# Kernel tuning notes

Measured on AMD Instinct MI355X. Metric: run time of the kernel, lower is better.

The kernel has to match this reference:

```python
import jax, jax.numpy as jnp
import numpy as np

STRIDE = 1
PAD = 1


def setup_inputs() -> dict:
    key = jax.random.key(0)
    k1, k2, k3 = jax.random.split(key, 3)
    # Single image (C_in, H, W) as in the original unbatched HETensor list layout
    x = jax.random.normal(k1, (256, 512, 512), dtype=jnp.float32)
    # Weights in HWIO layout (kh, kw, C_in, C_out) matching load_weights' expected shape
    W = jax.random.normal(k2, (3, 3, 256, 256), dtype=jnp.float32) * 0.02
    b = jax.random.normal(k3, (256,), dtype=jnp.float32)
    return {"x": x, "W": W, "b": b}


def reference(x, W, b):
    # Zero-pad then convolve; out_h = ceil((H + 2*PAD - kh + 1)/STRIDE) == lax conv output for stride 1
    out = jax.lax.conv_general_dilated(
        x[None],                      # [1, C_in, H, W]
        W,                            # [kh, kw, C_in, C_out]
        window_strides=(STRIDE, STRIDE),
        padding=[(PAD, PAD), (PAD, PAD)],
        dimension_numbers=("NCHW", "HWIO", "NCHW"),
    )
    return out[0] + b[:, None, None]  # [C_out, H, W]
```

## Files before the change

### kernel.cpp

```cpp
#include <hip/hip_runtime.h>
#include <hip/hip_bf16.h>


typedef __attribute__((ext_vector_type(8))) short bf16x8;
typedef __attribute__((ext_vector_type(4))) float floatx4;

#define HWSZ 262144
#define CIN  256
#define HH   512
#define WWD  512

__device__ __forceinline__ void async_copy16(const void* g, void* l) {
  __builtin_amdgcn_global_load_lds(
      (const __attribute__((address_space(1))) void*)g,
      (__attribute__((address_space(3))) void*)l, 16, 0, 0);
}

__global__ __launch_bounds__(256) void convert_x(
    const float* __restrict__ x, __hip_bfloat16* __restrict__ xt)
{
  const int b = blockIdx.x;
  const int h = b >> 1;
  const int w = ((b & 1) << 8) + threadIdx.x;
  const float* xp = x + (size_t)h * WWD + w;
#pragma unroll 2
  for (int cg = 0; cg < 32; ++cg) {
    const float* s = xp + (size_t)(cg << 3) * HWSZ;
    unsigned int q[4];
#pragma unroll
    for (int k = 0; k < 4; ++k) {
      float f0 = s[(size_t)(2 * k) * HWSZ];
      float f1 = s[(size_t)(2 * k + 1) * HWSZ];
      __hip_bfloat16 b0 = __float2bfloat16(f0);
      __hip_bfloat16 b1 = __float2bfloat16(f1);
      q[k] = (unsigned int)*(const unsigned short*)&b0 |
             ((unsigned int)*(const unsigned short*)&b1 << 16);
    }
    uint4 v;
    v.x = q[0]; v.y = q[1]; v.z = q[2]; v.w = q[3];
    *(uint4*)&xt[(((size_t)h * 32 + cg) << 12) + ((size_t)w << 3)] = v;
  }
}

__global__ __launch_bounds__(256) void convert_w(
    const float* __restrict__ Wf, __hip_bfloat16* __restrict__ wt,
    __hip_bfloat16* __restrict__ zb)
{
  const int idx = blockIdx.x * 256 + threadIdx.x;
  const int ci = idx & 255;
  const int co = (idx >> 8) & 255;
  const int kk = idx >> 16;
  wt[(((size_t)(kk * 32 + (ci >> 3)) * 256 + co) << 3) + (ci & 7)] =
      __float2bfloat16(Wf[((size_t)(kk * 256 + ci) << 8) + co]);
  if (idx < 64) zb[idx] = __float2bfloat16(0.0f);
}

__global__ __launch_bounds__(256, 3) void conv_mfma(
    const __hip_bfloat16* __restrict__ xt,
    const __hip_bfloat16* __restrict__ wt,
    const float* __restrict__ bias,
    float* __restrict__ out,
    const __hip_bfloat16* __restrict__ zb)
{
  __shared__ __align__(16) __hip_bfloat16 As[3 * 128 * 32];
  __shared__ __align__(16) __hip_bfloat16 Bs[130 * 32];

  const int b     = blockIdx.x;
  const int xcd   = b & 7;
  const int local = b >> 3;
  const int h     = (xcd << 6) + (local >> 3);
  const int rem   = local & 7;
  const int cot   = rem >> 2;
  const int wti   = rem & 3;
  const int w0   = wti << 7;
  const int co0  = cot << 7;
  const int t    = threadIdx.x;
  const int lane = t & 63;
  const int wave = t >> 6;
  const int wm   = wave & 1;
  const int wn   = wave >> 1;
  const int mcol = lane & 15;
  const int krow = lane >> 4;


  floatx4 acc[4][4];
#pragma unroll
  for (int mi = 0; mi < 4; ++mi)
#pragma unroll
    for (int ni = 0; ni < 4; ++ni) {
      floatx4 z = {0.f, 0.f, 0.f, 0.f};
      acc[mi][ni] = z;
    }

  for (int kh = 0; kh < 3; ++kh) {
    const int hp = h + kh - 1;
    const bool hok = (unsigned)hp < (unsigned)HH;
    const __hip_bfloat16* xrow = xt + ((size_t)hp << 17);

    for (int ci0 = 0; ci0 < CIN; ci0 += 32) {
      const int cg0 = ci0 >> 3;
      __syncthreads();
#pragma unroll
      for (int rnd = 0; rnd < 6; ++rnd) {
        int c  = rnd * 256 + t;
        int kw = c >> 9;
        int m  = (c >> 2) & 127;
        int j  = c & 3;
        int js = j ^ ((m >> 1) & 3);
        const __hip_bfloat16* g =
            wt + (((size_t)((kh * 3 + kw) * 32 + cg0 + js)) << 11) + ((co0 + m) << 3);
        async_copy16(g, &As[c << 3]);
      }
#pragma unroll
      for (int rnd = 0; rnd < 2; ++rnd) {
        int c = rnd * 256 + t;
        int r = c >> 2;
        int j = c & 3;
        int js = j ^ ((r >> 1) & 3);
        int wp = w0 - 1 + r;
        const __hip_bfloat16* g = (hok && (unsigned)wp < (unsigned)WWD)
            ? xrow + ((size_t)(cg0 + js) << 12) + (wp << 3)
            : zb + (js << 3);
        async_copy16(g, &Bs[c << 3]);
      }
      if (t < 8) {
        int c = 512 + t;
        int r = c >> 2;
        int j = c & 3;
        int js = j ^ ((r >> 1) & 3);
        int wp = w0 - 1 + r;
        const __hip_bfloat16* g = (hok && (unsigned)wp < (unsigned)WWD)
            ? xrow + ((size_t)(cg0 + js) << 12) + (wp << 3)
            : zb + (js << 3);
        async_copy16(g, &Bs[c << 3]);
      }
      __syncthreads();

#pragma unroll
      for (int kw = 0; kw < 3; ++kw) {
        bf16x8 af[4], bfr[4];
#pragma unroll
        for (int mi = 0; mi < 4; ++mi) {
          int row = wm * 64 + mi * 16 + mcol;
          af[mi] = *(const bf16x8*)&As[(kw << 12) + (row << 5) +
                                       ((krow ^ ((row >> 1) & 3)) << 3)];
        }
#pragma unroll
        for (int ni = 0; ni < 4; ++ni) {
          int r = wn * 64 + ni * 16 + mcol + kw;
          bfr[ni] = *(const bf16x8*)&Bs[(r << 5) +
                                        ((krow ^ ((r >> 1) & 3)) << 3)];
        }
#pragma unroll
        for (int mi = 0; mi < 4; ++mi)
#pragma unroll
          for (int ni = 0; ni < 4; ++ni)
            acc[mi][ni] = __builtin_amdgcn_mfma_f32_16x16x32_bf16(
                af[mi], bfr[ni], acc[mi][ni], 0, 0, 0);
      }
    }
  }

  const size_t outrow = (size_t)h * WWD;
#pragma unroll
  for (int mi = 0; mi < 4; ++mi) {
#pragma unroll
    for (int r = 0; r < 4; ++r) {
      int co = co0 + wm * 64 + mi * 16 + krow * 4 + r;
      float bv = bias[co];
      float* op = out + (size_t)co * HWSZ + outrow + w0 + wn * 64 + mcol;
#pragma unroll
      for (int ni = 0; ni < 4; ++ni)
        op[ni * 16] = acc[mi][ni][r] + bv;
    }
  }
}

__global__ __launch_bounds__(256) void conv_naive(
    const float* __restrict__ x, const float* __restrict__ Wf,
    const float* __restrict__ bias, float* __restrict__ out)
{
  size_t idx = (size_t)blockIdx.x * 256 + threadIdx.x;
  int w  = (int)(idx & 511);
  int h  = (int)((idx >> 9) & 511);
  int co = (int)(idx >> 18);
  float acc = bias[co];
  for (int kh = 0; kh < 3; ++kh) {
    int hp = h + kh - 1;
    if ((unsigned)hp >= 512u) continue;
    for (int kw = 0; kw < 3; ++kw) {
      int wp = w + kw - 1;
      if ((unsigned)wp >= 512u) continue;
      const float* wcol = Wf + ((size_t)(kh * 3 + kw) << 16) + co;
      const float* xpix = x + (size_t)hp * 512 + wp;
      for (int ci = 0; ci < 256; ++ci)
        acc += xpix[(size_t)ci * HWSZ] * wcol[(size_t)ci << 8];
    }
  }
  out[idx] = acc;
}

extern "C" void kernel_launch(void* const* d_in, const int* in_sizes, int n_in,
                              void* d_out, int out_size, void* d_ws, size_t ws_size,
                              hipStream_t stream) {
  const float* x    = (const float*)d_in[0];
  const float* Wf   = (const float*)d_in[1];
  const float* bias = (const float*)d_in[2];
  float* out = (float*)d_out;

  const size_t xt_bytes = (size_t)HH * WWD * CIN * 2;
  const size_t wt_bytes = (size_t)9 * 256 * 256 * 2;
  const size_t need = xt_bytes + wt_bytes + 256;

  if (ws_size >= need) {
    __hip_bfloat16* xt = (__hip_bfloat16*)d_ws;
    __hip_bfloat16* wt = (__hip_bfloat16*)((char*)d_ws + xt_bytes);
    __hip_bfloat16* zb = (__hip_bfloat16*)((char*)d_ws + xt_bytes + wt_bytes);
    convert_x<<<1024, 256, 0, stream>>>(x, xt);
    convert_w<<<2304, 256, 0, stream>>>(Wf, wt, zb);
    conv_mfma<<<4096, 256, 0, stream>>>(xt, wt, bias, out, zb);
  } else {
    conv_naive<<<262144, 256, 0, stream>>>(x, Wf, bias, out);
  }
}
```

Before: 809.4 us.

## Double-buffer conv MFMA LDS tiles and regroup bf16 layout into 32-channel chunks

Reworks the implicit-GEMM convolution so global-to-LDS async copies for the next (kh, channel-chunk) stage are issued while the current stage's MFMAs run, using two LDS buffers and one barrier per stage. The x and weight bf16 intermediate layouts are regrouped so each pixel/output channel stores 32 contiguous channels, which makes global loads contiguous. The two halo columns are now loaded directly into registers and patched into the B fragments rather than staged in LDS. LDS use doubles and occupancy is lowered to 2 blocks per CU, trading latency hiding through occupancy for explicit prefetch.

```diff
diff --git a/kernel.cpp b/kernel.cpp
--- a/kernel.cpp
+++ b/kernel.cpp
@@ -19,26 +19,33 @@
 __global__ __launch_bounds__(256) void convert_x(
     const float* __restrict__ x, __hip_bfloat16* __restrict__ xt)
 {
-  const int b = blockIdx.x;
-  const int h = b >> 1;
-  const int w = ((b & 1) << 8) + threadIdx.x;
-  const float* xp = x + (size_t)h * WWD + w;
+  const int b  = blockIdx.x;
+  const int h  = b >> 1;
+  const int wh = (b & 1) << 8;
+  const int t  = threadIdx.x;
+  const int q  = t >> 2;
+  const int j  = t & 3;
+  const float* xbase = x + (size_t)h * WWD;
 #pragma unroll 2
-  for (int cg = 0; cg < 32; ++cg) {
-    const float* s = xp + (size_t)(cg << 3) * HWSZ;
-    unsigned int q[4];
-#pragma unroll
-    for (int k = 0; k < 4; ++k) {
-      float f0 = s[(size_t)(2 * k) * HWSZ];
-      float f1 = s[(size_t)(2 * k + 1) * HWSZ];
-      __hip_bfloat16 b0 = __float2bfloat16(f0);
-      __hip_bfloat16 b1 = __float2bfloat16(f1);
-      q[k] = (unsigned int)*(const unsigned short*)&b0 |
-             ((unsigned int)*(const unsigned short*)&b1 << 16);
-    }
-    uint4 v;
-    v.x = q[0]; v.y = q[1]; v.z = q[2]; v.w = q[3];
-    *(uint4*)&xt[(((size_t)h * 32 + cg) << 12) + ((size_t)w << 3)] = v;
+  for (int cg4 = 0; cg4 < 8; ++cg4) {
+#pragma unroll
+    for (int pass = 0; pass < 4; ++pass) {
+      int w = wh + pass * 64 + q;
+      const float* s = xbase + (size_t)(cg4 * 32 + j * 8) * HWSZ + w;
+      unsigned int qw[4];
+#pragma unroll
+      for (int k = 0; k < 4; ++k) {
+        float f0 = s[(size_t)(2 * k) * HWSZ];
+        float f1 = s[(size_t)(2 * k + 1) * HWSZ];
+        __hip_bfloat16 b0 = __float2bfloat16(f0);
+        __hip_bfloat16 b1 = __float2bfloat16(f1);
+        qw[k] = (unsigned int)*(const unsigned short*)&b0 |
+                ((unsigned int)*(const unsigned short*)&b1 << 16);
+      }
+      uint4 v;
+      v.x = qw[0]; v.y = qw[1]; v.z = qw[2]; v.w = qw[3];
+      *(uint4*)&xt[(((size_t)h * 8 + cg4) << 14) + (w << 5) + (j << 3)] = v;
+    }
   }
 }
 
@@ -50,20 +57,20 @@
   const int ci = idx & 255;
   const int co = (idx >> 8) & 255;
   const int kk = idx >> 16;
-  wt[(((size_t)(kk * 32 + (ci >> 3)) * 256 + co) << 3) + (ci & 7)] =
+  wt[((((size_t)kk * 8 + (ci >> 5)) * 256 + co) << 5) + (ci & 31)] =
       __float2bfloat16(Wf[((size_t)(kk * 256 + ci) << 8) + co]);
   if (idx < 64) zb[idx] = __float2bfloat16(0.0f);
 }
 
-__global__ __launch_bounds__(256, 3) void conv_mfma(
+__global__ __launch_bounds__(256, 2) void conv_mfma(
     const __hip_bfloat16* __restrict__ xt,
     const __hip_bfloat16* __restrict__ wt,
     const float* __restrict__ bias,
     float* __restrict__ out,
     const __hip_bfloat16* __restrict__ zb)
 {
-  __shared__ __align__(16) __hip_bfloat16 As[3 * 128 * 32];
-  __shared__ __align__(16) __hip_bfloat16 Bs[130 * 32];
+  __shared__ __align__(16) __hip_bfloat16 As[2][3 * 128 * 32];
+  __shared__ __align__(16) __hip_bfloat16 Bs[2][128 * 32];
 
   const int b     = blockIdx.x;
   const int xcd   = b & 7;
@@ -82,6 +89,10 @@
   const int mcol = lane & 15;
   const int krow = lane >> 4;
 
+  const int  wL   = w0 - 1;
+  const int  wR   = w0 + 128;
+  const bool wLok = (wL >= 0);
+  const bool wRok = (wR < WWD);
 
   floatx4 acc[4][4];
 #pragma unroll
@@ -92,73 +103,87 @@
       acc[mi][ni] = z;
     }
 
-  for (int kh = 0; kh < 3; ++kh) {
-    const int hp = h + kh - 1;
+  auto STAGE = [&](int s, __hip_bfloat16* Ad, __hip_bfloat16* Bd,
+                   bf16x8* hl, bf16x8* hr) {
+    const int kh  = s >> 3;
+    const int cg4 = s & 7;
+    const int hp  = h + kh - 1;
     const bool hok = (unsigned)hp < (unsigned)HH;
-    const __hip_bfloat16* xrow = xt + ((size_t)hp << 17);
-
-    for (int ci0 = 0; ci0 < CIN; ci0 += 32) {
-      const int cg0 = ci0 >> 3;
-      __syncthreads();
-#pragma unroll
-      for (int rnd = 0; rnd < 6; ++rnd) {
-        int c  = rnd * 256 + t;
-        int kw = c >> 9;
-        int m  = (c >> 2) & 127;
-        int j  = c & 3;
-        int js = j ^ ((m >> 1) & 3);
-        const __hip_bfloat16* g =
-            wt + (((size_t)((kh * 3 + kw) * 32 + cg0 + js)) << 11) + ((co0 + m) << 3);
-        async_copy16(g, &As[c << 3]);
-      }
-#pragma unroll
-      for (int rnd = 0; rnd < 2; ++rnd) {
-        int c = rnd * 256 + t;
-        int r = c >> 2;
-        int j = c & 3;
-        int js = j ^ ((r >> 1) & 3);
-        int wp = w0 - 1 + r;
-        const __hip_bfloat16* g = (hok && (unsigned)wp < (unsigned)WWD)
-            ? xrow + ((size_t)(cg0 + js) << 12) + (wp << 3)
-            : zb + (js << 3);
-        async_copy16(g, &Bs[c << 3]);
-      }
-      if (t < 8) {
-        int c = 512 + t;
-        int r = c >> 2;
-        int j = c & 3;
-        int js = j ^ ((r >> 1) & 3);
-        int wp = w0 - 1 + r;
-        const __hip_bfloat16* g = (hok && (unsigned)wp < (unsigned)WWD)
-            ? xrow + ((size_t)(cg0 + js) << 12) + (wp << 3)
-            : zb + (js << 3);
-        async_copy16(g, &Bs[c << 3]);
-      }
-      __syncthreads();
-
-#pragma unroll
-      for (int kw = 0; kw < 3; ++kw) {
-        bf16x8 af[4], bfr[4];
-#pragma unroll
-        for (int mi = 0; mi < 4; ++mi) {
-          int row = wm * 64 + mi * 16 + mcol;
-          af[mi] = *(const bf16x8*)&As[(kw << 12) + (row << 5) +
-                                       ((krow ^ ((row >> 1) & 3)) << 3)];
-        }
-#pragma unroll
-        for (int ni = 0; ni < 4; ++ni) {
-          int r = wn * 64 + ni * 16 + mcol + kw;
-          bfr[ni] = *(const bf16x8*)&Bs[(r << 5) +
-                                        ((krow ^ ((r >> 1) & 3)) << 3)];
-        }
-#pragma unroll
-        for (int mi = 0; mi < 4; ++mi)
-#pragma unroll
-          for (int ni = 0; ni < 4; ++ni)
-            acc[mi][ni] = __builtin_amdgcn_mfma_f32_16x16x32_bf16(
-                af[mi], bfr[ni], acc[mi][ni], 0, 0, 0);
-      }
-    }
+    const __hip_bfloat16* xp = xt + (((size_t)hp * 8 + cg4) << 14);
+#pragma unroll
+    for (int rnd = 0; rnd < 6; ++rnd) {
+      int c  = rnd * 256 + t;
+      int kw = c >> 9;
+      int m  = (c >> 2) & 127;
+      int j  = c & 3;
+      int js = j ^ ((m >> 1) & 3);
+      const __hip_bfloat16* g =
+          wt + ((((size_t)(kh * 3 + kw) * 8 + cg4) * 256 + co0 + m) << 5) + (js << 3);
+      async_copy16(g, Ad + (c << 3));
+    }
+#pragma unroll
+    for (int rnd = 0; rnd < 2; ++rnd) {
+      int c = rnd * 256 + t;
+      int r = c >> 2;
+      int j = c & 3;
+      int js = j ^ ((r >> 1) & 3);
+      const __hip_bfloat16* g = hok ? xp + ((w0 + r) << 5) + (js << 3)
+                                    : zb + (js << 3);
+      async_copy16(g, Bd + (c << 3));
+    }
+    const __hip_bfloat16* gl = (hok && wLok) ? xp + (wL << 5) + (krow << 3) : zb;
+    const __hip_bfloat16* gr = (hok && wRok) ? xp + (wR << 5) + (krow << 3) : zb;
+    *hl = *(const bf16x8*)gl;
+    *hr = *(const bf16x8*)gr;
+  };
+
+  auto COMPUTE = [&](const __hip_bfloat16* A, const __hip_bfloat16* B,
+                     bf16x8 hl, bf16x8 hr) {
+#pragma unroll
+    for (int kw = 0; kw < 3; ++kw) {
+      bf16x8 af[4], bfr[4];
+#pragma unroll
+      for (int mi = 0; mi < 4; ++mi) {
+        int row = wm * 64 + mi * 16 + mcol;
+        af[mi] = *(const bf16x8*)&A[(kw << 12) + (row << 5) +
+                                    ((krow ^ ((row >> 1) & 3)) << 3)];
+      }
+#pragma unroll
+      for (int ni = 0; ni < 4; ++ni) {
+        int r  = wn * 64 + ni * 16 + mcol + kw - 1;
+        int rc = r & 127;
+        bfr[ni] = *(const bf16x8*)&B[(rc << 5) +
+                                     ((krow ^ ((rc >> 1) & 3)) << 3)];
+      }
+      if (kw == 0) {
+        bool c = (wn == 0) && (mcol == 0);
+        bfr[0] = c ? hl : bfr[0];
+      }
+      if (kw == 2) {
+        bool c = (wn == 1) && (mcol == 15);
+        bfr[3] = c ? hr : bfr[3];
+      }
+#pragma unroll
+      for (int mi = 0; mi < 4; ++mi)
+#pragma unroll
+        for (int ni = 0; ni < 4; ++ni)
+          acc[mi][ni] = __builtin_amdgcn_mfma_f32_16x16x32_bf16(
+              af[mi], bfr[ni], acc[mi][ni], 0, 0, 0);
+    }
+  };
+
+  bf16x8 hl0, hr0, hl1, hr1;
+  STAGE(0, As[0], Bs[0], &hl0, &hr0);
+  __syncthreads();
+
+  for (int ss = 0; ss < 12; ++ss) {
+    const int s = ss * 2;
+    STAGE(s + 1, As[1], Bs[1], &hl1, &hr1);
+    COMPUTE(As[0], Bs[0], hl0, hr0);
+    __syncthreads();
+    if (s + 2 < 24) STAGE(s + 2, As[0], Bs[0], &hl0, &hr0);
+    COMPUTE(As[1], Bs[1], hl1, hr1);
+    __syncthreads();
   }
 
   const size_t outrow = (size_t)h * WWD;
```

Measured after the change: 727.0 us. -10.2%, faster.

## Regroup bf16 staging layouts into 32-channel contiguous chunks

Applied to the files above, without the earlier changes.

Changes the intermediate bf16 layouts of the input and weights from 8-channel groups to 32-channel groups, so each pixel or output channel's 32 input channels for one K-step sit in 64 contiguous bytes. The conversion kernels and the conv kernel's async LDS load addressing are updated to match. Each async copy wave now reads fewer, larger contiguous segments from global memory, which should improve coalescing, at the cost of a slightly different store pattern in the conversion kernel.

```diff
diff --git a/kernel.cpp b/kernel.cpp
--- a/kernel.cpp
+++ b/kernel.cpp
@@ -19,26 +19,33 @@
 __global__ __launch_bounds__(256) void convert_x(
     const float* __restrict__ x, __hip_bfloat16* __restrict__ xt)
 {
-  const int b = blockIdx.x;
-  const int h = b >> 1;
-  const int w = ((b & 1) << 8) + threadIdx.x;
-  const float* xp = x + (size_t)h * WWD + w;
+  const int b  = blockIdx.x;
+  const int h  = b >> 1;
+  const int wh = (b & 1) << 8;
+  const int t  = threadIdx.x;
+  const int q  = t >> 2;
+  const int j  = t & 3;
+  const float* xbase = x + (size_t)h * WWD;
 #pragma unroll 2
-  for (int cg = 0; cg < 32; ++cg) {
-    const float* s = xp + (size_t)(cg << 3) * HWSZ;
-    unsigned int q[4];
-#pragma unroll
-    for (int k = 0; k < 4; ++k) {
-      float f0 = s[(size_t)(2 * k) * HWSZ];
-      float f1 = s[(size_t)(2 * k + 1) * HWSZ];
-      __hip_bfloat16 b0 = __float2bfloat16(f0);
-      __hip_bfloat16 b1 = __float2bfloat16(f1);
-      q[k] = (unsigned int)*(const unsigned short*)&b0 |
-             ((unsigned int)*(const unsigned short*)&b1 << 16);
-    }
-    uint4 v;
-    v.x = q[0]; v.y = q[1]; v.z = q[2]; v.w = q[3];
-    *(uint4*)&xt[(((size_t)h * 32 + cg) << 12) + ((size_t)w << 3)] = v;
+  for (int cg4 = 0; cg4 < 8; ++cg4) {
+#pragma unroll
+    for (int pass = 0; pass < 4; ++pass) {
+      int w = wh + pass * 64 + q;
+      const float* s = xbase + (size_t)(cg4 * 32 + j * 8) * HWSZ + w;
+      unsigned int qw[4];
+#pragma unroll
+      for (int k = 0; k < 4; ++k) {
+        float f0 = s[(size_t)(2 * k) * HWSZ];
+        float f1 = s[(size_t)(2 * k + 1) * HWSZ];
+        __hip_bfloat16 b0 = __float2bfloat16(f0);
+        __hip_bfloat16 b1 = __float2bfloat16(f1);
+        qw[k] = (unsigned int)*(const unsigned short*)&b0 |
+                ((unsigned int)*(const unsigned short*)&b1 << 16);
+      }
+      uint4 v;
+      v.x = qw[0]; v.y = qw[1]; v.z = qw[2]; v.w = qw[3];
+      *(uint4*)&xt[(((size_t)h * 8 + cg4) << 14) + (w << 5) + (j << 3)] = v;
+    }
   }
 }
 
@@ -50,7 +57,7 @@
   const int ci = idx & 255;
   const int co = (idx >> 8) & 255;
   const int kk = idx >> 16;
-  wt[(((size_t)(kk * 32 + (ci >> 3)) * 256 + co) << 3) + (ci & 7)] =
+  wt[((((size_t)kk * 8 + (ci >> 5)) * 256 + co) << 5) + (ci & 31)] =
       __float2bfloat16(Wf[((size_t)(kk * 256 + ci) << 8) + co]);
   if (idx < 64) zb[idx] = __float2bfloat16(0.0f);
 }
@@ -82,7 +89,6 @@
   const int mcol = lane & 15;
   const int krow = lane >> 4;
 
-
   floatx4 acc[4][4];
 #pragma unroll
   for (int mi = 0; mi < 4; ++mi)
@@ -93,12 +99,11 @@
     }
 
   for (int kh = 0; kh < 3; ++kh) {
-    const int hp = h + kh - 1;
+    const int hp  = h + kh - 1;
     const bool hok = (unsigned)hp < (unsigned)HH;
-    const __hip_bfloat16* xrow = xt + ((size_t)hp << 17);
-
-    for (int ci0 = 0; ci0 < CIN; ci0 += 32) {
-      const int cg0 = ci0 >> 3;
+
+    for (int cg4 = 0; cg4 < 8; ++cg4) {
+      const __hip_bfloat16* xp = xt + (((size_t)hp * 8 + cg4) << 14);
       __syncthreads();
 #pragma unroll
       for (int rnd = 0; rnd < 6; ++rnd) {
@@ -108,7 +113,7 @@
         int j  = c & 3;
         int js = j ^ ((m >> 1) & 3);
         const __hip_bfloat16* g =
-            wt + (((size_t)((kh * 3 + kw) * 32 + cg0 + js)) << 11) + ((co0 + m) << 3);
+            wt + ((((size_t)(kh * 3 + kw) * 8 + cg4) * 256 + co0 + m) << 5) + (js << 3);
         async_copy16(g, &As[c << 3]);
       }
 #pragma unroll
@@ -119,7 +124,7 @@
         int js = j ^ ((r >> 1) & 3);
         int wp = w0 - 1 + r;
         const __hip_bfloat16* g = (hok && (unsigned)wp < (unsigned)WWD)
-            ? xrow + ((size_t)(cg0 + js) << 12) + (wp << 3)
+            ? xp + (wp << 5) + (js << 3)
             : zb + (js << 3);
         async_copy16(g, &Bs[c << 3]);
       }
@@ -130,7 +135,7 @@
         int js = j ^ ((r >> 1) & 3);
         int wp = w0 - 1 + r;
         const __hip_bfloat16* g = (hok && (unsigned)wp < (unsigned)WWD)
-            ? xrow + ((size_t)(cg0 + js) << 12) + (wp << 3)
+            ? xp + (wp << 5) + (js << 3)
             : zb + (js << 3);
         async_copy16(g, &Bs[c << 3]);
       }
```

Result: faster. 699.9 us (-13.5%).
